# Optimization experiments

Hardware: AMD Instinct MI355X
Metric: run time of the kernel (lower is better)

## Reference

```python
import jax, jax.numpy as jnp
import numpy as np

COST_LABELS = 2.0
COST_BBOX = 5.0
COST_GIOU = 2.0
NUM_HEADS = 7
NUM_CLASSES = 16


def setup_inputs() -> dict:
    key = jax.random.key(0)
    k0, k1, k2, k3 = jax.random.split(key, 4)
    bs, nq, nt = 16, 900, 100
    return {
        "pred_logits": jax.random.normal(k0, (NUM_HEADS, bs, nq, NUM_CLASSES), jnp.float32),
        "pred_boxes": jax.random.uniform(k1, (bs, nq, 4), jnp.float32),
        "tgt_boxes": jax.random.uniform(k2, (bs, nt, 4), jnp.float32),
        "tgt_labels": jax.random.randint(k3, (NUM_HEADS, bs, nt), 0, NUM_CLASSES),
    }


def box_cxcywh_to_xyxy(b):
    cx, cy, w, h = jnp.split(b, 4, axis=-1)
    return jnp.concatenate([cx - 0.5 * w, cy - 0.5 * h, cx + 0.5 * w, cy + 0.5 * h], axis=-1)


def generalized_box_iou(a, b):
    # a: [N,4] xyxy, b: [M,4] xyxy -> [N,M]
    area_a = (a[:, 2] - a[:, 0]) * (a[:, 3] - a[:, 1])
    area_b = (b[:, 2] - b[:, 0]) * (b[:, 3] - b[:, 1])
    lt = jnp.maximum(a[:, None, :2], b[None, :, :2])
    rb = jnp.minimum(a[:, None, 2:], b[None, :, 2:])
    wh = jnp.clip(rb - lt, 0.0)
    inter = wh[..., 0] * wh[..., 1]
    union = area_a[:, None] + area_b[None, :] - inter
    iou = inter / union
    lt_e = jnp.minimum(a[:, None, :2], b[None, :, :2])
    rb_e = jnp.maximum(a[:, None, 2:], b[None, :, 2:])
    wh_e = jnp.clip(rb_e - lt_e, 0.0)
    area = wh_e[..., 0] * wh_e[..., 1]
    return iou - (area - union) / area


@jax.jit
def compute_cost(pred_logits, pred_boxes, tgt_boxes, tgt_labels):
    bs, nq, _ = pred_boxes.shape
    out_bbox = pred_boxes.reshape(-1, 4)   # [N,4] cxcywh
    tgt_bbox = tgt_boxes.reshape(-1, 4)    # [M,4] cxcywh
    # L1 cdist
    cost_bbox = jnp.sum(jnp.abs(out_bbox[:, None, :] - tgt_bbox[None, :, :]), axis=-1)
    cost_giou = -generalized_box_iou(box_cxcywh_to_xyxy(out_bbox), box_cxcywh_to_xyxy(tgt_bbox))
    # label cost: sum over the 7 heads of -sigmoid(logits)[:, tgt_ids]
    probs = jax.nn.sigmoid(pred_logits.reshape(NUM_HEADS, -1, NUM_CLASSES))  # [7,N,C]
    ids = tgt_labels.reshape(NUM_HEADS, -1)                                   # [7,M]
    cost_labels = jnp.zeros_like(cost_bbox)
    for h in range(NUM_HEADS):  # small fixed loop, avoids a [7,N,M] intermediate
        cost_labels = cost_labels - probs[h][:, ids[h]]
    C = COST_BBOX * cost_bbox + COST_LABELS * cost_labels + COST_GIOU * cost_giou
    return C.reshape(bs, nq, -1)  # [bs, nq, bs*nt]


def _lsa(cost):
    """Jonker-Volgenant shortest augmenting path. cost: [r,c] with r<=c.
    Returns row2col: optimal column for each row (minimizes total cost)."""
    cost = np.asarray(cost, dtype=np.float64)
    r, c = cost.shape
    u = np.zeros(r + 1)
    v = np.zeros(c + 1)
    p = np.zeros(c + 1, np.int64)    # p[j] = row matched to column j (1-indexed)
    way = np.zeros(c + 1, np.int64)
    for i in range(1, r + 1):
        p[0] = i
        j0 = 0
        minv = np.full(c + 1, np.inf)
        used = np.zeros(c + 1, bool)
        while True:
            used[j0] = True
            i0 = p[j0]
            free = np.nonzero(~used)[0]  # unused columns (1..c)
            cur = cost[i0 - 1, free - 1] - u[i0] - v[free]
            better = cur < minv[free]
            minv[free] = np.where(better, cur, minv[free])
            way[free[better]] = j0
            k = np.argmin(minv[free])
            j1 = free[k]
            delta = minv[free][k]
            u[p[used]] += delta
            v[used] -= delta
            minv[free] -= delta
            j0 = j1
            if p[j0] == 0:
                break
        while j0:
            j1 = way[j0]
            p[j0] = p[j1]
            j0 = j1
    row2col = np.full(r, -1, np.int64)
    for j in range(1, c + 1):
        if p[j] > 0:
            row2col[p[j] - 1] = j - 1
    return row2col


def reference(pred_logits, pred_boxes, tgt_boxes, tgt_labels):
    C = compute_cost(pred_logits, pred_boxes, tgt_boxes, tgt_labels)  # [bs, nq, bs*nt]
    bs, nq, M = C.shape
    nt = M // bs
    Cn = np.asarray(C)
    out = np.zeros((bs, 2, nt), np.int64)
    for b in range(bs):
        sub = Cn[b, :, b * nt:(b + 1) * nt]  # [nq, nt] per-image block (mimics C.split(sizes))
        t2p = _lsa(sub.T)                    # for each target, its matched prediction
        order = np.argsort(t2p, kind="stable")  # scipy returns row indices sorted
        out[b, 0] = t2p[order]  # index_i: selected predictions (sorted)
        out[b, 1] = order       # index_j: corresponding targets
    return jnp.asarray(out)
```

## Files before the change

kernel.cpp:

```cpp
#include <hip/hip_runtime.h>
#include <hip/hip_bf16.h>
#include <math.h>

#define NQ 900
#define NT 100
#define BS 16
#define NH 7
#define NC 16
#define NSLOT 16
#define MAXTREE 8192

__global__ __launch_bounds__(256) void sig_transpose_kernel(const float* __restrict__ logits,
                                                            float* __restrict__ probsT) {
    const int hb = blockIdx.x;
    const float* src = logits + (size_t)hb * NQ * NC;
    float* dst = probsT + (size_t)hb * NC * NQ;
    __shared__ float tile[NC][NQ + 1];
    for (int e = threadIdx.x; e < NQ * NC; e += 256) {
        int q = e >> 4, c = e & 15;
        float x = src[e];
        tile[c][q] = 1.0f / (1.0f + expf(-x));
    }
    __syncthreads();
    for (int c = 0; c < NC; ++c)
        for (int q = threadIdx.x; q < NQ; q += 256)
            dst[c * NQ + q] = tile[c][q];
}

__global__ __launch_bounds__(256) void cost_kernel_bt(const float4* __restrict__ pboxes4,
                                                      const float4* __restrict__ tboxes4,
                                                      const int*    __restrict__ tlabels,
                                                      const float*  __restrict__ probsT,
                                                      float* __restrict__ costT) {
    const int bt = blockIdx.x;
    const int b = bt / NT, t = bt % NT;

    const float* prow[NH];
    #pragma unroll
    for (int h = 0; h < NH; ++h) {
        int lab = tlabels[(h * BS + b) * NT + t];
        prow[h] = probsT + (size_t)((h * BS + b) * NC + lab) * NQ;
    }

    float4 tb = tboxes4[b * NT + t];
    float tx = tb.x, ty = tb.y, tw = tb.z, th = tb.w;
    float bx0 = tx - 0.5f * tw, by0 = ty - 0.5f * th;
    float bx1 = tx + 0.5f * tw, by1 = ty + 0.5f * th;
    float areaB = (bx1 - bx0) * (by1 - by0);

    for (int q = threadIdx.x; q < NQ; q += 256) {
        float4 pb = pboxes4[b * NQ + q];
        float px = pb.x, py = pb.y, pw = pb.z, ph = pb.w;

        float cost_bbox = fabsf(px - tx) + fabsf(py - ty) + fabsf(pw - tw) + fabsf(ph - th);

        float ax0 = px - 0.5f * pw, ay0 = py - 0.5f * ph;
        float ax1 = px + 0.5f * pw, ay1 = py + 0.5f * ph;
        float areaA = (ax1 - ax0) * (ay1 - ay0);
        float ltx = fmaxf(ax0, bx0), lty = fmaxf(ay0, by0);
        float rbx = fminf(ax1, bx1), rby = fminf(ay1, by1);
        float iw = fmaxf(rbx - ltx, 0.f), ih = fmaxf(rby - lty, 0.f);
        float inter = iw * ih;
        float uni = areaA + areaB - inter;
        float iou = inter / uni;
        float ex0 = fminf(ax0, bx0), ey0 = fminf(ay0, by0);
        float ex1 = fmaxf(ax1, bx1), ey1 = fmaxf(ay1, by1);
        float ew = fmaxf(ex1 - ex0, 0.f), eh = fmaxf(ey1 - ey0, 0.f);
        float earea = ew * eh;
        float giou = iou - (earea - uni) / earea;

        float ssum = 0.f;
        #pragma unroll
        for (int h = 0; h < NH; ++h) ssum += prow[h][q];

        costT[(b * NT + t) * NQ + q] = 5.0f * cost_bbox - 2.0f * ssum - 2.0f * giou;
    }
}

__global__ void cost_kernel_fb(const float* __restrict__ logits,
                               const float* __restrict__ pboxes,
                               const float* __restrict__ tboxes,
                               const int*   __restrict__ tlabels,
                               float* __restrict__ costT) {
    int id = blockIdx.x * blockDim.x + threadIdx.x;
    if (id >= BS * NT * NQ) return;
    int q = id % NQ;
    int t = (id / NQ) % NT;
    int b = id / (NQ * NT);

    const float* pb = pboxes + (b * NQ + q) * 4;
    const float* tb = tboxes + (b * NT + t) * 4;
    float px = pb[0], py = pb[1], pw = pb[2], ph = pb[3];
    float tx = tb[0], ty = tb[1], tw = tb[2], th = tb[3];

    float cost_bbox = fabsf(px - tx) + fabsf(py - ty) + fabsf(pw - tw) + fabsf(ph - th);

    float ax0 = px - 0.5f * pw, ay0 = py - 0.5f * ph;
    float ax1 = px + 0.5f * pw, ay1 = py + 0.5f * ph;
    float bx0 = tx - 0.5f * tw, by0 = ty - 0.5f * th;
    float bx1 = tx + 0.5f * tw, by1 = ty + 0.5f * th;
    float areaA = (ax1 - ax0) * (ay1 - ay0);
    float areaB = (bx1 - bx0) * (by1 - by0);
    float ltx = fmaxf(ax0, bx0), lty = fmaxf(ay0, by0);
    float rbx = fminf(ax1, bx1), rby = fminf(ay1, by1);
    float iw = fmaxf(rbx - ltx, 0.f), ih = fmaxf(rby - lty, 0.f);
    float inter = iw * ih;
    float uni = areaA + areaB - inter;
    float iou = inter / uni;
    float ex0 = fminf(ax0, bx0), ey0 = fminf(ay0, by0);
    float ex1 = fmaxf(ax1, bx1), ey1 = fmaxf(ay1, by1);
    float ew = fmaxf(ex1 - ex0, 0.f), eh = fmaxf(ey1 - ey0, 0.f);
    float earea = ew * eh;
    float giou = iou - (earea - uni) / earea;

    float ssum = 0.f;
    #pragma unroll
    for (int h = 0; h < NH; ++h) {
        int lab = tlabels[(h * BS + b) * NT + t];
        float x = logits[((h * BS + b) * NQ + q) * NC + lab];
        ssum += 1.0f / (1.0f + expf(-x));
    }

    costT[(b * NT + t) * NQ + q] = 5.0f * cost_bbox - 2.0f * ssum - 2.0f * giou;
}

__global__ __launch_bounds__(64) void lsa_kernel(const float* __restrict__ costT,
                                                 int* __restrict__ out) {
    const int b = blockIdx.x;
    const int lane = threadIdx.x;
    const float* cost = costT + b * NT * NQ;

    __shared__ double u_s[NT + 1];
    __shared__ int p_s[NQ + 1];
    __shared__ int way2[NSLOT][64];
    __shared__ int p_w[NQ + 1];
    __shared__ int jmin_s[NT];
    __shared__ int listA[NT];
    __shared__ int r2c[NT];
    __shared__ int cnt_s;

    for (int j = lane; j <= NQ; j += 64) {
        p_s[j] = 0;
        p_w[j] = 0x7fffffff;
    }
    __syncthreads();

    bool lostA = false, lostB = false;
    #pragma unroll
    for (int pass = 0; pass < 2; ++pass) {
        int r = pass * 64 + lane;
        if (r < NT) {
            const float4* row4 = (const float4*)(cost + (size_t)r * NQ);
            float m0 = INFINITY, m1f = INFINITY, m2f = INFINITY, m3f = INFINITY;
            int i0 = 0, i1 = 0, i2 = 0, i3 = 0;
            #pragma unroll 5
            for (int q4 = 0; q4 < NQ / 4; ++q4) {
                float4 cv = row4[q4];
                if (cv.x < m0)  { m0 = cv.x;  i0 = 4 * q4; }
                if (cv.y < m1f) { m1f = cv.y; i1 = 4 * q4 + 1; }
                if (cv.z < m2f) { m2f = cv.z; i2 = 4 * q4 + 2; }
                if (cv.w < m3f) { m3f = cv.w; i3 = 4 * q4 + 3; }
            }
            float mv = m0; int mj = i0;
            if (m1f < mv || (m1f == mv && i1 < mj)) { mv = m1f; mj = i1; }
            if (m2f < mv || (m2f == mv && i2 < mj)) { mv = m2f; mj = i2; }
            if (m3f < mv || (m3f == mv && i3 < mj)) { mv = m3f; mj = i3; }
            u_s[r + 1] = (double)mv;
            jmin_s[r] = mj;
            atomicMin(&p_w[mj + 1], r + 1);
        }
    }
    __syncthreads();

    {
        int rA = lane;
        int j = jmin_s[rA] + 1;
        if (p_w[j] == rA + 1) p_s[j] = rA + 1;
        else lostA = true;
    }
    if (lane < NT - 64) {
        int rB = 64 + lane;
        int j = jmin_s[rB] + 1;
        if (p_w[j] == rB + 1) p_s[j] = rB + 1;
        else lostB = true;
    }
    unsigned long long mA = __ballot(lostA);
    unsigned long long mB = __ballot(lostB);
    if (lane == 0) {
        int n = 0;
        unsigned long long m = mA;
        while (m) { int l = __ffsll((unsigned long long)m) - 1; listA[n++] = l + 1; m &= m - 1; }
        m = mB;
        while (m) { int l = __ffsll((unsigned long long)m) - 1; listA[n++] = 64 + l + 1; m &= m - 1; }
        cnt_s = n;
    }
    __syncthreads();
    const int nfree = cnt_s;

    double v[NSLOT], minv[NSLOT], upreg[NSLOT], dreg[NSLOT];
    int preg[NSLOT];
    const unsigned invalid = (lane <= 32) ? 0u : 0xF000u;
    #pragma unroll
    for (int s = 0; s < NSLOT; ++s) {
        v[s] = 0.0; dreg[s] = 0.0;
        int pr = 0;
        if (!((invalid >> s) & 1u)) {
            int j = 1 + 4 * lane + 256 * (s >> 2) + (s & 3);
            pr = p_s[j];
        }
        preg[s] = pr;
        upreg[s] = (pr > 0) ? u_s[pr] : 0.0;
    }
    __syncthreads();

    for (int ii = 0; ii < nfree; ++ii) {
        const int i = listA[ii];
        #pragma unroll
        for (int s = 0; s < NSLOT; ++s) minv[s] = INFINITY;
        unsigned used = invalid;
        int j0 = 0;
        int i0 = i;
        double u_i0 = u_s[i];
        const double u_root = u_i0;
        double d0 = 0.0;
        double deltaf = 0.0;
        int guard = 0;

        while (guard++ < MAXTREE) {
            if (j0 != 0) {
                int idx = j0 - 1;
                if (lane == ((idx >> 2) & 63)) {
                    int slot = ((idx >> 8) << 2) | (idx & 3);
                    used |= (1u << slot);
                    #pragma unroll
                    for (int s = 0; s < NSLOT; ++s)
                        if (s == slot) dreg[s] = d0;
                }
            }

            const float4* crow4 = (const float4*)(cost + (size_t)(i0 - 1) * NQ);
            float4 c4[4];
            #pragma unroll
            for (int kc = 0; kc < 3; ++kc) c4[kc] = crow4[lane + 64 * kc];
            c4[3] = (lane <= 32) ? crow4[lane + 192] : make_float4(0.f, 0.f, 0.f, 0.f);

            const double duv = d0 - u_i0;
            double bv = INFINITY;
            int bj = 2048, bs = 0;
            #pragma unroll
            for (int kc = 0; kc < 4; ++kc) {
                #pragma unroll
                for (int e = 0; e < 4; ++e) {
                    const int s = 4 * kc + e;
                    if (!((used >> s) & 1u)) {
                        float cf = (e == 0) ? c4[kc].x : (e == 1) ? c4[kc].y
                                 : (e == 2) ? c4[kc].z : c4[kc].w;
                        double cand = ((double)cf + duv) - v[s];
                        int j = 1 + 4 * lane + 256 * kc + e;
                        if (cand < minv[s]) { minv[s] = cand; way2[s][lane] = j0; }
                        if (minv[s] < bv) { bv = minv[s]; bj = j; bs = s; }
                    }
                }
            }
            double vmin = bv;
            #pragma unroll
            for (int off = 1; off < 64; off <<= 1)
                vmin = fmin(vmin, __shfl_xor(vmin, off));
            unsigned long long tied = __ballot(bv == vmin);
            int wl = __ffsll((unsigned long long)tied) - 1;
            int jwin = __shfl(bj, wl);

            int pb = 0; double ub = 0.0;
            #pragma unroll
            for (int s = 0; s < NSLOT; ++s)
                if (s == bs) { pb = preg[s]; ub = upreg[s]; }
            int i0n = __shfl(pb, wl);
            double u_n = __shfl(ub, wl);

            j0 = jwin;
            d0 = vmin;
            if (i0n == 0) { deltaf = vmin; break; }
            i0 = i0n;
            u_i0 = u_n;
        }

        __syncthreads();
        #pragma unroll
        for (int s = 0; s < NSLOT; ++s) {
            if (((used >> s) & 1u) && !((invalid >> s) & 1u)) {
                v[s] += (dreg[s] - deltaf);
                u_s[preg[s]] = upreg[s] + (deltaf - dreg[s]);
            }
        }
        if (lane == 0) u_s[i] = u_root + deltaf;
        __syncthreads();
        if (lane == 0) {
            int j = j0;
            while (j) {
                int idx = j - 1;
                int ol = (idx >> 2) & 63;
                int sl = ((idx >> 8) << 2) | (idx & 3);
                int jw = way2[sl][ol];
                p_s[j] = (jw == 0) ? i : p_s[jw];
                j = jw;
            }
        }
        __syncthreads();
        #pragma unroll
        for (int s = 0; s < NSLOT; ++s) {
            if (!((invalid >> s) & 1u)) {
                int j = 1 + 4 * lane + 256 * (s >> 2) + (s & 3);
                if (((used >> s) & 1u) || (j == j0)) {
                    int pr = p_s[j];
                    preg[s] = pr;
                    upreg[s] = (pr > 0) ? u_s[pr] : 0.0;
                }
            }
        }
    }

    __syncthreads();
    for (int j = 1 + lane; j <= NQ; j += 64) {
        int pi = p_s[j];
        if (pi > 0) r2c[pi - 1] = j - 1;
    }
    __syncthreads();
    for (int t = lane; t < NT; t += 64) {
        int ccol = r2c[t];
        int rank = 0;
        for (int tt = 0; tt < NT; ++tt) rank += (r2c[tt] < ccol) ? 1 : 0;
        out[b * 2 * NT + rank] = ccol;
        out[b * 2 * NT + NT + rank] = t;
    }
}

extern "C" void kernel_launch(void* const* d_in, const int* in_sizes, int n_in,
                              void* d_out, int out_size, void* d_ws, size_t ws_size,
                              hipStream_t stream) {
    const float* logits  = (const float*)d_in[0];
    const float* pboxes  = (const float*)d_in[1];
    const float* tboxes  = (const float*)d_in[2];
    const int*   tlabels = (const int*)d_in[3];
    int* out = (int*)d_out;
    float* costT = (float*)d_ws;

    const size_t costT_elems  = (size_t)BS * NT * NQ;
    const size_t probsT_elems = (size_t)NH * BS * NC * NQ;
    const size_t need = (costT_elems + probsT_elems) * sizeof(float);

    if (ws_size >= need) {
        float* probsT = costT + costT_elems;
        sig_transpose_kernel<<<NH * BS, 256, 0, stream>>>(logits, probsT);
        cost_kernel_bt<<<BS * NT, 256, 0, stream>>>((const float4*)pboxes,
                                                    (const float4*)tboxes, tlabels, probsT, costT);
    } else {
        const int total = BS * NT * NQ;
        cost_kernel_fb<<<(total + 255) / 256, 256, 0, stream>>>(logits, pboxes, tboxes, tlabels, costT);
    }
    lsa_kernel<<<BS, 64, 0, stream>>>(costT, out);
}
```

Before: 121.6 us.

## Fuse sigmoid into cost kernel and tree-reduce per-lane minimum in LSA

Drops the separate sigmoid/transpose kernel and probsT workspace. The cost kernel now gathers logits directly and applies the sigmoid inline, which saves one launch and a round trip through global memory but makes the logit reads strided. In the LSA kernel, the serial per-slot running minimum becomes a log-depth tree reduction over the 16 slots. It also precomputes column indices per slot and resets minv when a column is marked used.

```diff
diff --git a/kernel.cpp b/kernel.cpp
--- a/kernel.cpp
+++ b/kernel.cpp
@@ -10,37 +10,17 @@
 #define NSLOT 16
 #define MAXTREE 8192
 
-__global__ __launch_bounds__(256) void sig_transpose_kernel(const float* __restrict__ logits,
-                                                            float* __restrict__ probsT) {
-    const int hb = blockIdx.x;
-    const float* src = logits + (size_t)hb * NQ * NC;
-    float* dst = probsT + (size_t)hb * NC * NQ;
-    __shared__ float tile[NC][NQ + 1];
-    for (int e = threadIdx.x; e < NQ * NC; e += 256) {
-        int q = e >> 4, c = e & 15;
-        float x = src[e];
-        tile[c][q] = 1.0f / (1.0f + expf(-x));
-    }
-    __syncthreads();
-    for (int c = 0; c < NC; ++c)
-        for (int q = threadIdx.x; q < NQ; q += 256)
-            dst[c * NQ + q] = tile[c][q];
-}
-
-__global__ __launch_bounds__(256) void cost_kernel_bt(const float4* __restrict__ pboxes4,
-                                                      const float4* __restrict__ tboxes4,
-                                                      const int*    __restrict__ tlabels,
-                                                      const float*  __restrict__ probsT,
-                                                      float* __restrict__ costT) {
+__global__ __launch_bounds__(256) void cost_kernel(const float*  __restrict__ logits,
+                                                   const float4* __restrict__ pboxes4,
+                                                   const float4* __restrict__ tboxes4,
+                                                   const int*    __restrict__ tlabels,
+                                                   float* __restrict__ costT) {
     const int bt = blockIdx.x;
     const int b = bt / NT, t = bt % NT;
 
-    const float* prow[NH];
+    int lab[NH];
     #pragma unroll
-    for (int h = 0; h < NH; ++h) {
-        int lab = tlabels[(h * BS + b) * NT + t];
-        prow[h] = probsT + (size_t)((h * BS + b) * NC + lab) * NQ;
-    }
+    for (int h = 0; h < NH; ++h) lab[h] = tlabels[(h * BS + b) * NT + t];
 
     float4 tb = tboxes4[b * NT + t];
     float tx = tb.x, ty = tb.y, tw = tb.z, th = tb.w;
@@ -71,57 +51,13 @@
 
         float ssum = 0.f;
         #pragma unroll
-        for (int h = 0; h < NH; ++h) ssum += prow[h][q];
+        for (int h = 0; h < NH; ++h) {
+            float x = logits[(size_t)((h * BS + b) * NQ + q) * NC + lab[h]];
+            ssum += 1.0f / (1.0f + expf(-x));
+        }
 
         costT[(b * NT + t) * NQ + q] = 5.0f * cost_bbox - 2.0f * ssum - 2.0f * giou;
     }
-}
-
-__global__ void cost_kernel_fb(const float* __restrict__ logits,
-                               const float* __restrict__ pboxes,
-                               const float* __restrict__ tboxes,
-                               const int*   __restrict__ tlabels,
-                               float* __restrict__ costT) {
-    int id = blockIdx.x * blockDim.x + threadIdx.x;
-    if (id >= BS * NT * NQ) return;
-    int q = id % NQ;
-    int t = (id / NQ) % NT;
-    int b = id / (NQ * NT);
-
-    const float* pb = pboxes + (b * NQ + q) * 4;
-    const float* tb = tboxes + (b * NT + t) * 4;
-    float px = pb[0], py = pb[1], pw = pb[2], ph = pb[3];
-    float tx = tb[0], ty = tb[1], tw = tb[2], th = tb[3];
-
-    float cost_bbox = fabsf(px - tx) + fabsf(py - ty) + fabsf(pw - tw) + fabsf(ph - th);
-
-    float ax0 = px - 0.5f * pw, ay0 = py - 0.5f * ph;
-    float ax1 = px + 0.5f * pw, ay1 = py + 0.5f * ph;
-    float bx0 = tx - 0.5f * tw, by0 = ty - 0.5f * th;
-    float bx1 = tx + 0.5f * tw, by1 = ty + 0.5f * th;
-    float areaA = (ax1 - ax0) * (ay1 - ay0);
-    float areaB = (bx1 - bx0) * (by1 - by0);
-    float ltx = fmaxf(ax0, bx0), lty = fmaxf(ay0, by0);
-    float rbx = fminf(ax1, bx1), rby = fminf(ay1, by1);
-    float iw = fmaxf(rbx - ltx, 0.f), ih = fmaxf(rby - lty, 0.f);
-    float inter = iw * ih;
-    float uni = areaA + areaB - inter;
-    float iou = inter / uni;
-    float ex0 = fminf(ax0, bx0), ey0 = fminf(ay0, by0);
-    float ex1 = fmaxf(ax1, bx1), ey1 = fmaxf(ay1, by1);
-    float ew = fmaxf(ex1 - ex0, 0.f), eh = fmaxf(ey1 - ey0, 0.f);
-    float earea = ew * eh;
-    float giou = iou - (earea - uni) / earea;
-
-    float ssum = 0.f;
-    #pragma unroll
-    for (int h = 0; h < NH; ++h) {
-        int lab = tlabels[(h * BS + b) * NT + t];
-        float x = logits[((h * BS + b) * NQ + q) * NC + lab];
-        ssum += 1.0f / (1.0f + expf(-x));
-    }
-
-    costT[(b * NT + t) * NQ + q] = 5.0f * cost_bbox - 2.0f * ssum - 2.0f * giou;
 }
 
 __global__ __launch_bounds__(64) void lsa_kernel(const float* __restrict__ costT,
@@ -199,15 +135,14 @@
 
     double v[NSLOT], minv[NSLOT], upreg[NSLOT], dreg[NSLOT];
     int preg[NSLOT];
+    int jof[NSLOT];
     const unsigned invalid = (lane <= 32) ? 0u : 0xF000u;
     #pragma unroll
     for (int s = 0; s < NSLOT; ++s) {
         v[s] = 0.0; dreg[s] = 0.0;
+        jof[s] = 1 + 4 * lane + 256 * (s >> 2) + (s & 3);
         int pr = 0;
-        if (!((invalid >> s) & 1u)) {
-            int j = 1 + 4 * lane + 256 * (s >> 2) + (s & 3);
-            pr = p_s[j];
-        }
+        if (!((invalid >> s) & 1u)) pr = p_s[jof[s]];
         preg[s] = pr;
         upreg[s] = (pr > 0) ? u_s[pr] : 0.0;
     }
@@ -216,7 +151,8 @@
     for (int ii = 0; ii < nfree; ++ii) {
         const int i = listA[ii];
         #pragma unroll
-        for (int s = 0; s < NSLOT; ++s) minv[s] = INFINITY;
+        for (int s = 0; s < NSLOT; ++s)
+            minv[s] = ((invalid >> s) & 1u) ? INFINITY : INFINITY;
         unsigned used = invalid;
         int j0 = 0;
         int i0 = i;
@@ -234,7 +170,7 @@
                     used |= (1u << slot);
                     #pragma unroll
                     for (int s = 0; s < NSLOT; ++s)
-                        if (s == slot) dreg[s] = d0;
+                        if (s == slot) { dreg[s] = d0; minv[s] = INFINITY; }
                 }
             }
 
@@ -245,8 +181,6 @@
             c4[3] = (lane <= 32) ? crow4[lane + 192] : make_float4(0.f, 0.f, 0.f, 0.f);
 
             const double duv = d0 - u_i0;
-            double bv = INFINITY;
-            int bj = 2048, bs = 0;
             #pragma unroll
             for (int kc = 0; kc < 4; ++kc) {
                 #pragma unroll
@@ -256,12 +190,26 @@
                         float cf = (e == 0) ? c4[kc].x : (e == 1) ? c4[kc].y
                                  : (e == 2) ? c4[kc].z : c4[kc].w;
                         double cand = ((double)cf + duv) - v[s];
-                        int j = 1 + 4 * lane + 256 * kc + e;
                         if (cand < minv[s]) { minv[s] = cand; way2[s][lane] = j0; }
-                        if (minv[s] < bv) { bv = minv[s]; bj = j; bs = s; }
                     }
                 }
             }
+
+            double tm[NSLOT]; int tj[NSLOT];
+            #pragma unroll
+            for (int s = 0; s < NSLOT; ++s) { tm[s] = minv[s]; tj[s] = jof[s]; }
+            #pragma unroll
+            for (int st = 8; st >= 1; st >>= 1) {
+                #pragma unroll
+                for (int s = 0; s < 8; ++s) {
+                    if (s < st) {
+                        if (tm[s + st] < tm[s]) { tm[s] = tm[s + st]; tj[s] = tj[s + st]; }
+                    }
+                }
+            }
+            const double bv = tm[0];
+            const int bj = tj[0];
+
             double vmin = bv;
             #pragma unroll
             for (int off = 1; off < 64; off <<= 1)
@@ -270,6 +218,7 @@
             int wl = __ffsll((unsigned long long)tied) - 1;
             int jwin = __shfl(bj, wl);
 
+            int bs = (((bj - 1) >> 8) << 2) | ((bj - 1) & 3);
             int pb = 0; double ub = 0.0;
             #pragma unroll
             for (int s = 0; s < NSLOT; ++s)
@@ -309,9 +258,8 @@
         #pragma unroll
         for (int s = 0; s < NSLOT; ++s) {
             if (!((invalid >> s) & 1u)) {
-                int j = 1 + 4 * lane + 256 * (s >> 2) + (s & 3);
-                if (((used >> s) & 1u) || (j == j0)) {
-                    int pr = p_s[j];
+                if (((used >> s) & 1u) || (jof[s] == j0)) {
+                    int pr = p_s[jof[s]];
                     preg[s] = pr;
                     upreg[s] = (pr > 0) ? u_s[pr] : 0.0;
                 }
@@ -344,18 +292,7 @@
     int* out = (int*)d_out;
     float* costT = (float*)d_ws;
 
-    const size_t costT_elems  = (size_t)BS * NT * NQ;
-    const size_t probsT_elems = (size_t)NH * BS * NC * NQ;
-    const size_t need = (costT_elems + probsT_elems) * sizeof(float);
-
-    if (ws_size >= need) {
-        float* probsT = costT + costT_elems;
-        sig_transpose_kernel<<<NH * BS, 256, 0, stream>>>(logits, probsT);
-        cost_kernel_bt<<<BS * NT, 256, 0, stream>>>((const float4*)pboxes,
-                                                    (const float4*)tboxes, tlabels, probsT, costT);
-    } else {
-        const int total = BS * NT * NQ;
-        cost_kernel_fb<<<(total + 255) / 256, 256, 0, stream>>>(logits, pboxes, tboxes, tlabels, costT);
-    }
+    cost_kernel<<<BS * NT, 256, 0, stream>>>(logits, (const float4*)pboxes,
+                                             (const float4*)tboxes, tlabels, costT);
     lsa_kernel<<<BS, 64, 0, stream>>>(costT, out);
 }
```

After: 123.9 us. No clear change (+1.9%).
